# Kernel tuning notes

Hardware: AMD Instinct MI355X
Metric: run time of the kernel (lower is better)

## Reference

```python
import jax, jax.numpy as jnp
import numpy as np

DIM_Q = 512
DIM_K = 512
DIM_V = 512
NUM_HEADS = 8
B, NQ, NK = 4, 2048, 2048


def _linear_init(key, d_in, d_out):
    kw, kb = jax.random.split(key)
    bound = 1.0 / np.sqrt(d_in)
    W = jax.random.uniform(kw, (d_in, d_out), minval=-bound, maxval=bound, dtype=jnp.float32)
    b = jax.random.uniform(kb, (d_out,), minval=-bound, maxval=bound, dtype=jnp.float32)
    return W, b


def setup_inputs() -> dict:
    key = jax.random.key(0)
    ks = jax.random.split(key, 6)
    Q = jax.random.normal(ks[0], (B, NQ, DIM_Q), dtype=jnp.float32)
    K = jax.random.normal(ks[1], (B, NK, DIM_K), dtype=jnp.float32)
    Wq, bq = _linear_init(ks[2], DIM_Q, DIM_V)
    Wk, bk = _linear_init(ks[3], DIM_K, DIM_V)
    Wv, bv = _linear_init(ks[4], DIM_K, DIM_V)
    Wo, bo = _linear_init(ks[5], DIM_V, DIM_V)
    ln0_g = jnp.ones((DIM_V,), jnp.float32)
    ln0_b = jnp.zeros((DIM_V,), jnp.float32)
    ln1_g = jnp.ones((DIM_V,), jnp.float32)
    ln1_b = jnp.zeros((DIM_V,), jnp.float32)
    return {"Q": Q, "K": K, "Wq": Wq, "bq": bq, "Wk": Wk, "bk": bk,
            "Wv": Wv, "bv": bv, "Wo": Wo, "bo": bo,
            "ln0_g": ln0_g, "ln0_b": ln0_b, "ln1_g": ln1_g, "ln1_b": ln1_b}


def _layer_norm(x, g, b, eps=1e-5):
    mu = jnp.mean(x, axis=-1, keepdims=True)
    var = jnp.mean(jnp.square(x - mu), axis=-1, keepdims=True)
    return (x - mu) * jax.lax.rsqrt(var + eps) * g + b


def reference(Q, K, Wq, bq, Wk, bk, Wv, bv, Wo, bo, ln0_g, ln0_b, ln1_g, ln1_b):
    h = NUM_HEADS
    dh = DIM_V // h
    q = Q @ Wq + bq                      # [B, NQ, DIM_V]
    k = K @ Wk + bk                      # [B, NK, DIM_V]
    v = K @ Wv + bv                      # [B, NK, DIM_V]
    qh = q.reshape(B, NQ, h, dh)
    kh = k.reshape(B, NK, h, dh)
    vh = v.reshape(B, NK, h, dh)
    # NOTE: faithful to original — scale by sqrt(dim_V), not sqrt(head_dim)
    scores = jnp.einsum('bqhd,bkhd->bhqk', qh, kh) / jnp.sqrt(jnp.float32(DIM_V))
    A = jax.nn.softmax(scores, axis=-1)  # [B, h, NQ, NK]
    o = jnp.einsum('bhqk,bkhd->bqhd', A, vh) + qh
    H = o.reshape(B, NQ, DIM_V)          # residual with projected Q
    H = _layer_norm(H, ln0_g, ln0_b)
    H = H + jax.nn.relu(H @ Wo + bo)
    H = _layer_norm(H, ln1_g, ln1_b)
    return H
```

## Files before the change

### kernel.cpp

```cpp
#include <hip/hip_runtime.h>

typedef float f32x4 __attribute__((ext_vector_type(4)));
typedef float f32x16 __attribute__((ext_vector_type(16)));
typedef __bf16 bf16x8 __attribute__((ext_vector_type(8)));
typedef unsigned short u16;
typedef unsigned int u32;
typedef u16 u16x8 __attribute__((ext_vector_type(8)));
typedef u16 u16x4 __attribute__((ext_vector_type(4)));
typedef u32 u32x4 __attribute__((ext_vector_type(4)));

#define SCALE2F (0.044194173824159216f * 1.4426950408889634f)
#define UNSCALE (1.0f / SCALE2F)

__device__ __forceinline__ u16 f2bf(float x){ return __builtin_bit_cast(u16, (__bf16)x); }
__device__ __forceinline__ float bf2f(u16 h){ unsigned u = ((unsigned)h) << 16; return __builtin_bit_cast(float, u); }
__device__ __forceinline__ int swz(int r, int byteInRow){ return (r*128 + byteInRow) ^ ((r & 7) << 4); }
__device__ __forceinline__ void gload16(const void* g, void* l) {
  __builtin_amdgcn_global_load_lds(
      (const __attribute__((address_space(1))) void*)g,
      (__attribute__((address_space(3))) void*)l, 16, 0, 0);
}
__device__ __forceinline__ u32 cvtpk(float lo, float hi_) {
  u32 r;
  asm("v_cvt_pk_bf16_f32 %0, %1, %2" : "=v"(r) : "v"(lo), "v"(hi_));
  return r;
}
__device__ __forceinline__ void swap32(u32 &a, u32 &b) {
  asm("v_permlane32_swap_b32 %0, %1" : "+v"(a), "+v"(b));
}

#define MFMA(a,b,c)   __builtin_amdgcn_mfma_f32_16x16x32_bf16((a),(b),(c),0,0,0)
#define MFMA32(a,b,c) __builtin_amdgcn_mfma_f32_32x32x16_bf16((a),(b),(c),0,0,0)

__global__ __launch_bounds__(256) void wprep_k(
    const float* __restrict__ W0, const float* __restrict__ W1,
    const float* __restrict__ W2, const float* __restrict__ W3,
    u16* __restrict__ wt)
{
  __shared__ float tile[64][68];
  const float* Ws[4] = {W0, W1, W2, W3};
  const float* W = Ws[blockIdx.z];
  const float sc = (blockIdx.z == 0) ? SCALE2F : 1.0f;
  u16* out = wt + (size_t)blockIdx.z * 512 * 512;
  int k0 = blockIdx.x * 64, n0 = blockIdx.y * 64;
  int t = threadIdx.x;
  #pragma unroll
  for (int i = 0; i < 2; ++i) {
    int c = t + i*256; int r = c >> 3, k8 = c & 7;
    const float* src = W + (size_t)(k0 + r)*512 + n0 + k8*8;
    *(f32x4*)&tile[r][k8*8]     = *(const f32x4*)src;
    *(f32x4*)&tile[r][k8*8 + 4] = *(const f32x4*)(src + 4);
  }
  __syncthreads();
  #pragma unroll
  for (int i = 0; i < 2; ++i) {
    int c = t + i*256; int r = c >> 3, k8 = c & 7;
    u16x8 h;
    #pragma unroll
    for (int j = 0; j < 8; ++j) h[j] = f2bf(tile[k8*8 + j][r] * sc);
    *(u16x8*)(out + (size_t)(n0 + r)*512 + k0 + k8*8) = h;
  }
}

__global__ __launch_bounds__(512) void proj2_k(
    const float* __restrict__ Qin, const float* __restrict__ Kin,
    const u16* __restrict__ wt,
    const float* __restrict__ bq, const float* __restrict__ bk, const float* __restrict__ bv,
    u16* __restrict__ qbuf, u16* __restrict__ kbuf, u16* __restrict__ vt)
{
  __shared__ __align__(16) u16 lA[2][64*64];
  __shared__ __align__(16) u16 lB0[2][128*64];
  __shared__ __align__(16) u16 lB1[2][128*64];
  int z = blockIdx.z;
  const float* A     = z ? Kin : Qin;
  const u16*   Bt0   = wt + (size_t)(z ? 1 : 0) * 262144;
  const u16*   Bt1   = wt + (size_t)2 * 262144;
  const float* bias0 = z ? bk : bq;
  const float bscale = z ? 1.0f : SCALE2F;
  int row0 = blockIdx.x * 64, col0 = blockIdx.y * 128;
  int t = threadIdx.x, lane = t & 63, wid = t >> 6;
  int wr = wid >> 2, wc = wid & 3;
  int l15 = lane & 15, lg = lane >> 4;
  int ar = t >> 3, ak8 = t & 7;
  int br = t >> 3;
  int bsrc = (((t & 7) << 4) ^ ((br & 7) << 4)) >> 1;
  const float* Arow = A + (size_t)row0 * 512;
  const u16*   B0row = Bt0 + (size_t)col0 * 512;
  const u16*   B1row = Bt1 + (size_t)col0 * 512;

  f32x4 acc0[2][2] = {}, acc1[2][2] = {};

  #pragma unroll
  for (int i = 0; i < 2; ++i)
    gload16(B0row + (size_t)(br + i*64)*512 + bsrc, (char*)lB0[0] + i*8192 + t*16);
  if (z) {
    #pragma unroll
    for (int i = 0; i < 2; ++i)
      gload16(B1row + (size_t)(br + i*64)*512 + bsrc, (char*)lB1[0] + i*8192 + t*16);
  }
  {
    const float* src = Arow + (size_t)ar*512 + ak8*8;
    f32x4 x0 = *(const f32x4*)src;
    f32x4 x1 = *(const f32x4*)(src + 4);
    u16x8 h;
    #pragma unroll
    for (int j = 0; j < 4; ++j) { h[j] = f2bf(x0[j]); h[j+4] = f2bf(x1[j]); }
    *(u16x8*)((char*)lA[0] + swz(ar, ak8*16)) = h;
  }
  __syncthreads();

  int cur = 0;
  for (int k0 = 0; k0 < 512; k0 += 64) {
    bool pf = (k0 + 64 < 512);
    f32x4 px0, px1;
    if (pf) {
      #pragma unroll
      for (int i = 0; i < 2; ++i)
        gload16(B0row + (size_t)(br + i*64)*512 + k0 + 64 + bsrc, (char*)lB0[cur^1] + i*8192 + t*16);
      if (z) {
        #pragma unroll
        for (int i = 0; i < 2; ++i)
          gload16(B1row + (size_t)(br + i*64)*512 + k0 + 64 + bsrc, (char*)lB1[cur^1] + i*8192 + t*16);
      }
      const float* src = Arow + (size_t)ar*512 + k0 + 64 + ak8*8;
      px0 = *(const f32x4*)src;
      px1 = *(const f32x4*)(src + 4);
    }
    const char* lAc = (const char*)lA[cur];
    const char* lB0c = (const char*)lB0[cur];
    const char* lB1c = (const char*)lB1[cur];
    #pragma unroll
    for (int ks = 0; ks < 2; ++ks) {
      bf16x8 af[2], b0f[2], b1f[2];
      #pragma unroll
      for (int m = 0; m < 2; ++m)
        af[m] = *(const bf16x8*)(lAc + swz(wr*32 + m*16 + l15, ks*64 + lg*16));
      #pragma unroll
      for (int n = 0; n < 2; ++n) {
        int rb = wc*32 + n*16 + l15;
        b0f[n] = *(const bf16x8*)(lB0c + swz(rb, ks*64 + lg*16));
        if (z) b1f[n] = *(const bf16x8*)(lB1c + swz(rb, ks*64 + lg*16));
      }
      #pragma unroll
      for (int m = 0; m < 2; ++m)
        #pragma unroll
        for (int n = 0; n < 2; ++n) {
          acc0[m][n] = MFMA(af[m], b0f[n], acc0[m][n]);
          if (z) acc1[m][n] = MFMA(af[m], b1f[n], acc1[m][n]);
        }
    }
    if (pf) {
      u16x8 h;
      #pragma unroll
      for (int j = 0; j < 4; ++j) { h[j] = f2bf(px0[j]); h[j+4] = f2bf(px1[j]); }
      *(u16x8*)((char*)lA[cur^1] + swz(ar, ak8*16)) = h;
    }
    __syncthreads();
    cur ^= 1;
  }

  u16* out0 = z ? kbuf : qbuf;
  #pragma unroll
  for (int m = 0; m < 2; ++m) {
    int rowg = row0 + wr*32 + m*16 + lg*4;
    #pragma unroll
    for (int n = 0; n < 2; ++n) {
      int colg = col0 + wc*32 + n*16 + l15;
      float bvv = bias0[colg] * bscale;
      #pragma unroll
      for (int r = 0; r < 4; ++r)
        out0[(size_t)(rowg + r)*512 + colg] = f2bf(acc0[m][n][r] + bvv);
    }
  }
  if (z) {
    #pragma unroll
    for (int m = 0; m < 2; ++m) {
      int rowg = row0 + wr*32 + m*16 + lg*4;
      int b = rowg >> 11, ntok = rowg & 2047;
      #pragma unroll
      for (int n = 0; n < 2; ++n) {
        int colg = col0 + wc*32 + n*16 + l15;
        float bvv = bv[colg];
        u16x4 hv;
        #pragma unroll
        for (int r = 0; r < 4; ++r) hv[r] = f2bf(acc1[m][n][r] + bvv);
        *(u16x4*)(vt + ((size_t)b*512 + colg)*2048 + ntok) = hv;
      }
    }
  }
}

__global__ __launch_bounds__(512) void gemmo_k(
    const u16* __restrict__ A, const u16* __restrict__ Bt,
    const float* __restrict__ bias, u16* __restrict__ outb,
    const u16* __restrict__ resid)
{
  __shared__ __align__(16) u16 lA[2][64*64];
  __shared__ __align__(16) u16 lB[2][128*64];
  int row0 = blockIdx.x * 64, col0 = blockIdx.y * 128;
  int t = threadIdx.x, lane = t & 63, wid = t >> 6;
  int wr = wid >> 2, wc = wid & 3;
  int l15 = lane & 15, lg = lane >> 4;
  int ar = t >> 3;
  int asrc = (((t & 7) << 4) ^ ((ar & 7) << 4)) >> 1;
  const u16* Arow = A + (size_t)row0 * 512;
  const u16* Brow = Bt + (size_t)col0 * 512;
  f32x4 acc[2][2] = {};

  gload16(Arow + (size_t)ar*512 + asrc, (char*)lA[0] + t*16);
  #pragma unroll
  for (int i = 0; i < 2; ++i)
    gload16(Brow + (size_t)(ar + i*64)*512 + asrc, (char*)lB[0] + i*8192 + t*16);
  __syncthreads();

  int cur = 0;
  for (int k0 = 0; k0 < 512; k0 += 64) {
    if (k0 + 64 < 512) {
      gload16(Arow + (size_t)ar*512 + k0 + 64 + asrc, (char*)lA[cur^1] + t*16);
      #pragma unroll
      for (int i = 0; i < 2; ++i)
        gload16(Brow + (size_t)(ar + i*64)*512 + k0 + 64 + asrc, (char*)lB[cur^1] + i*8192 + t*16);
    }
    const char* lAc = (const char*)lA[cur];
    const char* lBc = (const char*)lB[cur];
    #pragma unroll
    for (int ks = 0; ks < 2; ++ks) {
      bf16x8 af[2], bfv[2];
      #pragma unroll
      for (int m = 0; m < 2; ++m)
        af[m] = *(const bf16x8*)(lAc + swz(wr*32 + m*16 + l15, ks*64 + lg*16));
      #pragma unroll
      for (int n = 0; n < 2; ++n)
        bfv[n] = *(const bf16x8*)(lBc + swz(wc*32 + n*16 + l15, ks*64 + lg*16));
      #pragma unroll
      for (int m = 0; m < 2; ++m)
        #pragma unroll
        for (int n = 0; n < 2; ++n)
          acc[m][n] = MFMA(af[m], bfv[n], acc[m][n]);
    }
    __syncthreads();
    cur ^= 1;
  }
  #pragma unroll
  for (int m = 0; m < 2; ++m) {
    int rowg = row0 + wr*32 + m*16 + lg*4;
    #pragma unroll
    for (int n = 0; n < 2; ++n) {
      int colg = col0 + wc*32 + n*16 + l15;
      float bvv = bias[colg];
      #pragma unroll
      for (int r = 0; r < 4; ++r) {
        size_t idx = (size_t)(rowg + r)*512 + colg;
        outb[idx] = f2bf(bf2f(resid[idx]) + fmaxf(acc[m][n][r] + bvv, 0.0f));
      }
    }
  }
}

__device__ __forceinline__ void mk_pb(const f32x16& s, float& ps, bf16x8& f0, bf16x8& f1) {
  float p[16];
  #pragma unroll
  for (int r = 0; r < 16; ++r) p[r] = __builtin_amdgcn_exp2f(s[r]);
  float t0 = (p[0] + p[1])  + (p[2] + p[3]);
  float t1 = (p[4] + p[5])  + (p[6] + p[7]);
  float t2 = (p[8] + p[9])  + (p[10] + p[11]);
  float t3 = (p[12] + p[13]) + (p[14] + p[15]);
  ps += (t0 + t1) + (t2 + t3);
  u32 a0 = cvtpk(p[0],  p[1]),  b0 = cvtpk(p[4],  p[5]);
  u32 a1 = cvtpk(p[2],  p[3]),  b1 = cvtpk(p[6],  p[7]);
  swap32(a0, b0); swap32(a1, b1);
  u32 a2 = cvtpk(p[8],  p[9]),  b2 = cvtpk(p[12], p[13]);
  u32 a3 = cvtpk(p[10], p[11]), b3 = cvtpk(p[14], p[15]);
  swap32(a2, b2); swap32(a3, b3);
  u32x4 w0 = {a0, a1, b0, b1};
  u32x4 w1 = {a2, a3, b2, b3};
  f0 = __builtin_bit_cast(bf16x8, w0);
  f1 = __builtin_bit_cast(bf16x8, w1);
}

__global__ __launch_bounds__(512, 4) void attn_k(
    const u16* __restrict__ qb, const u16* __restrict__ kb,
    const u16* __restrict__ vt, u16* __restrict__ ob)
{
  __shared__ __align__(16) char smem[65536];

  int t = threadIdx.x, lane = t & 63, wid = t >> 6;
  int bh = blockIdx.y, b = bh >> 3, h = bh & 7;
  int half = wid >> 2;
  int qw = wid & 3;
  int q0 = blockIdx.x * 128 + qw * 32;
  int l31 = lane & 31, hi = lane >> 5;

  const u16* kbase = kb + ((size_t)b*2048)*512 + h*64;
  const u16* vbase = vt + ((size_t)b*512 + h*64)*2048;

  int sr = t >> 3;
  int ssrc = ((t & 7) ^ (sr & 7)) << 3;

#define LKB(hf, bf) (smem + ((hf)*2 + (bf))*8192)
#define LVB(hf, bf) (smem + 32768 + ((hf)*2 + (bf))*8192)
#define STAGE(buf, off)                                                           \
  gload16(kbase + (size_t)((off) + sr)*512 + ssrc,        LKB(0,buf) + t*16);     \
  gload16(kbase + (size_t)((off) + 1024 + sr)*512 + ssrc, LKB(1,buf) + t*16);     \
  gload16(vbase + (size_t)sr*2048 + (off) + ssrc,         LVB(0,buf) + t*16);     \
  gload16(vbase + (size_t)sr*2048 + (off) + 1024 + ssrc,  LVB(1,buf) + t*16);

  bf16x8 aq[4];
  {
    const u16* qp = qb + ((size_t)(b*2048 + q0 + l31))*512 + h*64 + hi*8;
    #pragma unroll
    for (int ks = 0; ks < 4; ++ks) aq[ks] = *(const bf16x8*)(qp + ks*16);
  }

  f32x16 acc[2] = {};
  float ps = 0.0f;

  STAGE(0, 0);
  __syncthreads();

  int cur = 0;
  for (int i = 0; i < 16; ++i) {
    if (i + 1 < 16) { STAGE(cur^1, (i+1)*64); }
    const char* lKc = LKB(half, cur);
    const char* lVc = LVB(half, cur);
    bf16x8 pb[4];
    #pragma unroll
    for (int n = 0; n < 2; ++n) {
      f32x16 s = {};
      #pragma unroll
      for (int ks = 0; ks < 4; ++ks) {
        bf16x8 kf = *(const bf16x8*)(lKc + swz(n*32 + l31, ks*32 + hi*16));
        s = MFMA32(kf, aq[ks], s);
      }
      mk_pb(s, ps, pb[2*n], pb[2*n+1]);
    }
    #pragma unroll
    for (int m = 0; m < 2; ++m)
      #pragma unroll
      for (int ks = 0; ks < 4; ++ks) {
        bf16x8 vf = *(const bf16x8*)(lVc + swz(m*32 + l31, ks*32 + hi*16));
        acc[m] = MFMA32(vf, pb[ks], acc[m]);
      }
    __syncthreads();
    cur ^= 1;
  }
#undef STAGE

  ps += __shfl_xor(ps, 32, 64);
  float* cb = (float*)smem;
  if (half == 1) {
    float* dst = cb + qw * 2208;
    #pragma unroll
    for (int m = 0; m < 2; ++m)
      #pragma unroll
      for (int rq = 0; rq < 4; ++rq) {
        f32x4 v = {acc[m][rq*4], acc[m][rq*4+1], acc[m][rq*4+2], acc[m][rq*4+3]};
        *(f32x4*)(dst + l31*68 + m*32 + rq*8 + hi*4) = v;
      }
    if (hi == 0) dst[2176 + l31] = ps;
  }
  __syncthreads();
  if (half == 0) {
    const float* src = cb + qw * 2208;
    float inv = 1.0f / (ps + src[2176 + l31]);
    u16* obase = ob + ((size_t)(b*2048 + q0 + l31))*512 + h*64;
    const u16* qrb = qb + ((size_t)(b*2048 + q0 + l31))*512 + h*64;
    #pragma unroll
    for (int m = 0; m < 2; ++m)
      #pragma unroll
      for (int rq = 0; rq < 4; ++rq) {
        f32x4 other = *(const f32x4*)(src + l31*68 + m*32 + rq*8 + hi*4);
        u16x4 qr4 = *(const u16x4*)(qrb + m*32 + rq*8 + hi*4);
        u16x4 o4;
        #pragma unroll
        for (int e = 0; e < 4; ++e)
          o4[e] = f2bf((acc[m][rq*4 + e] + other[e])*inv + bf2f(qr4[e])*UNSCALE);
        *(u16x4*)(obase + m*32 + rq*8 + hi*4) = o4;
      }
  }
}

template<int OUT_BF16>
__global__ __launch_bounds__(256) void ln_k(
    const u16* __restrict__ x, const float* __restrict__ gam,
    const float* __restrict__ bet, float* __restrict__ yf, u16* __restrict__ yh)
{
  int t = threadIdx.x, lane = t & 63, w = t >> 6;
  size_t row = (size_t)blockIdx.x * 4 + w;
  u16x8 xv = *(const u16x8*)(x + row*512 + lane*8);
  float v[8];
  #pragma unroll
  for (int j = 0; j < 8; ++j) v[j] = bf2f(xv[j]);
  float s = 0.0f, ss = 0.0f;
  #pragma unroll
  for (int j = 0; j < 8; ++j) { s += v[j]; ss += v[j]*v[j]; }
  #pragma unroll
  for (int m = 1; m < 64; m <<= 1) { s += __shfl_xor(s, m, 64); ss += __shfl_xor(ss, m, 64); }
  float mu = s * (1.0f/512.0f);
  float var = ss * (1.0f/512.0f) - mu*mu;
  float rs = rsqrtf(var + 1e-5f);
  const float* gp = gam + lane*8;
  const float* bp = bet + lane*8;
  f32x4 g0 = *(const f32x4*)gp, g1 = *(const f32x4*)(gp + 4);
  f32x4 b0 = *(const f32x4*)bp, b1 = *(const f32x4*)(bp + 4);
  if (OUT_BF16) {
    u16x8 hv;
    #pragma unroll
    for (int j = 0; j < 4; ++j) {
      hv[j]   = f2bf((v[j]   - mu)*rs*g0[j] + b0[j]);
      hv[j+4] = f2bf((v[j+4] - mu)*rs*g1[j] + b1[j]);
    }
    *(u16x8*)(yh + row*512 + lane*8) = hv;
  } else {
    f32x4 o0, o1;
    #pragma unroll
    for (int j = 0; j < 4; ++j) {
      o0[j] = (v[j]   - mu)*rs*g0[j] + b0[j];
      o1[j] = (v[j+4] - mu)*rs*g1[j] + b1[j];
    }
    float* yp = yf + row*512 + lane*8;
    *(f32x4*)yp = o0;
    *(f32x4*)(yp + 4) = o1;
  }
}

extern "C" void kernel_launch(void* const* d_in, const int* in_sizes, int n_in,
                              void* d_out, int out_size, void* d_ws, size_t ws_size,
                              hipStream_t stream)
{
  const float* Q   = (const float*)d_in[0];
  const float* K   = (const float*)d_in[1];
  const float* Wq  = (const float*)d_in[2];
  const float* bq  = (const float*)d_in[3];
  const float* Wk  = (const float*)d_in[4];
  const float* bk  = (const float*)d_in[5];
  const float* Wv  = (const float*)d_in[6];
  const float* bv  = (const float*)d_in[7];
  const float* Wo  = (const float*)d_in[8];
  const float* bo  = (const float*)d_in[9];
  const float* g0  = (const float*)d_in[10];
  const float* b0  = (const float*)d_in[11];
  const float* g1  = (const float*)d_in[12];
  const float* b1  = (const float*)d_in[13];

  char* ws = (char*)d_ws;
  u16*   wt    = (u16*)(ws + 0);
  u16*   qbuf  = (u16*)(ws + (2u<<20));
  u16*   kbuf  = (u16*)(ws + (10u<<20));
  u16*   vt    = (u16*)(ws + (18u<<20));
  u16*   ob    = (u16*)(ws + (26u<<20));
  u16*   Hbuf  = (u16*)(ws + (34u<<20));
  u16*   Gb    = (u16*)(ws + (42u<<20));

  wprep_k<<<dim3(8, 8, 4), 256, 0, stream>>>(Wq, Wk, Wv, Wo, wt);
  proj2_k<<<dim3(128, 4, 2), 512, 0, stream>>>(Q, K, wt, bq, bk, bv, qbuf, kbuf, vt);
  attn_k<<<dim3(16, 32), 512, 0, stream>>>(qbuf, kbuf, vt, ob);
  ln_k<1><<<2048, 256, 0, stream>>>(ob, g0, b0, nullptr, Hbuf);
  gemmo_k<<<dim3(128, 4), 512, 0, stream>>>(Hbuf, wt + 3*262144, bo, Gb, Hbuf);
  ln_k<0><<<2048, 256, 0, stream>>>(Gb, g1, b1, (float*)d_out, nullptr);
}
```

Measured before the change: 97.91 us.

## Fuse LayerNorm0, output GEMM with ReLU residual, and LayerNorm1 into one kernel

```diff
diff --git a/kernel.cpp b/kernel.cpp
--- a/kernel.cpp
+++ b/kernel.cpp
@@ -190,73 +190,6 @@
   }
 }
 
-__global__ __launch_bounds__(512) void gemmo_k(
-    const u16* __restrict__ A, const u16* __restrict__ Bt,
-    const float* __restrict__ bias, u16* __restrict__ outb,
-    const u16* __restrict__ resid)
-{
-  __shared__ __align__(16) u16 lA[2][64*64];
-  __shared__ __align__(16) u16 lB[2][128*64];
-  int row0 = blockIdx.x * 64, col0 = blockIdx.y * 128;
-  int t = threadIdx.x, lane = t & 63, wid = t >> 6;
-  int wr = wid >> 2, wc = wid & 3;
-  int l15 = lane & 15, lg = lane >> 4;
-  int ar = t >> 3;
-  int asrc = (((t & 7) << 4) ^ ((ar & 7) << 4)) >> 1;
-  const u16* Arow = A + (size_t)row0 * 512;
-  const u16* Brow = Bt + (size_t)col0 * 512;
-  f32x4 acc[2][2] = {};
-
-  gload16(Arow + (size_t)ar*512 + asrc, (char*)lA[0] + t*16);
-  #pragma unroll
-  for (int i = 0; i < 2; ++i)
-    gload16(Brow + (size_t)(ar + i*64)*512 + asrc, (char*)lB[0] + i*8192 + t*16);
-  __syncthreads();
-
-  int cur = 0;
-  for (int k0 = 0; k0 < 512; k0 += 64) {
-    if (k0 + 64 < 512) {
-      gload16(Arow + (size_t)ar*512 + k0 + 64 + asrc, (char*)lA[cur^1] + t*16);
-      #pragma unroll
-      for (int i = 0; i < 2; ++i)
-        gload16(Brow + (size_t)(ar + i*64)*512 + k0 + 64 + asrc, (char*)lB[cur^1] + i*8192 + t*16);
-    }
-    const char* lAc = (const char*)lA[cur];
-    const char* lBc = (const char*)lB[cur];
-    #pragma unroll
-    for (int ks = 0; ks < 2; ++ks) {
-      bf16x8 af[2], bfv[2];
-      #pragma unroll
-      for (int m = 0; m < 2; ++m)
-        af[m] = *(const bf16x8*)(lAc + swz(wr*32 + m*16 + l15, ks*64 + lg*16));
-      #pragma unroll
-      for (int n = 0; n < 2; ++n)
-        bfv[n] = *(const bf16x8*)(lBc + swz(wc*32 + n*16 + l15, ks*64 + lg*16));
-      #pragma unroll
-      for (int m = 0; m < 2; ++m)
-        #pragma unroll
-        for (int n = 0; n < 2; ++n)
-          acc[m][n] = MFMA(af[m], bfv[n], acc[m][n]);
-    }
-    __syncthreads();
-    cur ^= 1;
-  }
-  #pragma unroll
-  for (int m = 0; m < 2; ++m) {
-    int rowg = row0 + wr*32 + m*16 + lg*4;
-    #pragma unroll
-    for (int n = 0; n < 2; ++n) {
-      int colg = col0 + wc*32 + n*16 + l15;
-      float bvv = bias[colg];
-      #pragma unroll
-      for (int r = 0; r < 4; ++r) {
-        size_t idx = (size_t)(rowg + r)*512 + colg;
-        outb[idx] = f2bf(bf2f(resid[idx]) + fmaxf(acc[m][n][r] + bvv, 0.0f));
-      }
-    }
-  }
-}
-
 __device__ __forceinline__ void mk_pb(const f32x16& s, float& ps, bf16x8& f0, bf16x8& f1) {
   float p[16];
   #pragma unroll
@@ -380,47 +313,161 @@
   }
 }
 
-template<int OUT_BF16>
-__global__ __launch_bounds__(256) void ln_k(
-    const u16* __restrict__ x, const float* __restrict__ gam,
-    const float* __restrict__ bet, float* __restrict__ yf, u16* __restrict__ yh)
+__global__ __launch_bounds__(512) void tail_k(
+    const u16* __restrict__ ob, const u16* __restrict__ Bt,
+    const float* __restrict__ bo,
+    const float* __restrict__ g0, const float* __restrict__ b0,
+    const float* __restrict__ g1, const float* __restrict__ b1,
+    float* __restrict__ out)
 {
-  int t = threadIdx.x, lane = t & 63, w = t >> 6;
-  size_t row = (size_t)blockIdx.x * 4 + w;
-  u16x8 xv = *(const u16x8*)(x + row*512 + lane*8);
-  float v[8];
-  #pragma unroll
-  for (int j = 0; j < 8; ++j) v[j] = bf2f(xv[j]);
-  float s = 0.0f, ss = 0.0f;
-  #pragma unroll
-  for (int j = 0; j < 8; ++j) { s += v[j]; ss += v[j]*v[j]; }
-  #pragma unroll
-  for (int m = 1; m < 64; m <<= 1) { s += __shfl_xor(s, m, 64); ss += __shfl_xor(ss, m, 64); }
-  float mu = s * (1.0f/512.0f);
-  float var = ss * (1.0f/512.0f) - mu*mu;
-  float rs = rsqrtf(var + 1e-5f);
-  const float* gp = gam + lane*8;
-  const float* bp = bet + lane*8;
-  f32x4 g0 = *(const f32x4*)gp, g1 = *(const f32x4*)(gp + 4);
-  f32x4 b0 = *(const f32x4*)bp, b1 = *(const f32x4*)(bp + 4);
-  if (OUT_BF16) {
-    u16x8 hv;
+  __shared__ __align__(16) u16 lA[2][32*64];
+  __shared__ __align__(16) u16 lB[2][512*64];
+  __shared__ float mu0[32], rs0[32], mu1[32], rs1[32];
+  __shared__ float ps1[32][8], ss1[32][8];
+
+  int row0 = blockIdx.x * 32;
+  int t = threadIdx.x, lane = t & 63, wid = t >> 6;
+  int l15 = lane & 15, lg = lane >> 4;
+
+  {
+    int r = t >> 4, c0 = (t & 15) * 32;
+    const u16* xp = ob + (size_t)(row0 + r)*512 + c0;
+    float s = 0.0f, ss = 0.0f;
     #pragma unroll
     for (int j = 0; j < 4; ++j) {
-      hv[j]   = f2bf((v[j]   - mu)*rs*g0[j] + b0[j]);
-      hv[j+4] = f2bf((v[j+4] - mu)*rs*g1[j] + b1[j]);
-    }
-    *(u16x8*)(yh + row*512 + lane*8) = hv;
-  } else {
-    f32x4 o0, o1;
-    #pragma unroll
-    for (int j = 0; j < 4; ++j) {
-      o0[j] = (v[j]   - mu)*rs*g0[j] + b0[j];
-      o1[j] = (v[j+4] - mu)*rs*g1[j] + b1[j];
-    }
-    float* yp = yf + row*512 + lane*8;
-    *(f32x4*)yp = o0;
-    *(f32x4*)(yp + 4) = o1;
+      u16x8 v = *(const u16x8*)(xp + j*8);
+      #pragma unroll
+      for (int e = 0; e < 8; ++e) { float f = bf2f(v[e]); s += f; ss += f*f; }
+    }
+    #pragma unroll
+    for (int m = 1; m < 16; m <<= 1) { s += __shfl_xor(s, m, 64); ss += __shfl_xor(ss, m, 64); }
+    if ((t & 15) == 0) {
+      float mu = s * (1.0f/512.0f);
+      float var = ss * (1.0f/512.0f) - mu*mu;
+      mu0[r] = mu; rs0[r] = rsqrtf(var + 1e-5f);
+    }
+  }
+  __syncthreads();
+
+  int ar = t >> 3, ak8 = t & 7;
+  int br = t >> 3;
+  int bsrc = ((t & 7) ^ (br & 7)) << 3;
+
+  auto stageA = [&](int buf, int k0) {
+    if (t < 256) {
+      u16x8 x = *(const u16x8*)(ob + (size_t)(row0 + ar)*512 + k0 + ak8*8);
+      f32x4 gv0 = *(const f32x4*)(g0 + k0 + ak8*8);
+      f32x4 gv1 = *(const f32x4*)(g0 + k0 + ak8*8 + 4);
+      f32x4 bv0 = *(const f32x4*)(b0 + k0 + ak8*8);
+      f32x4 bv1 = *(const f32x4*)(b0 + k0 + ak8*8 + 4);
+      float mu = mu0[ar], rs = rs0[ar];
+      u16x8 h;
+      #pragma unroll
+      for (int j = 0; j < 4; ++j) {
+        h[j]   = f2bf((bf2f(x[j])   - mu)*rs*gv0[j] + bv0[j]);
+        h[j+4] = f2bf((bf2f(x[j+4]) - mu)*rs*gv1[j] + bv1[j]);
+      }
+      *(u16x8*)((char*)lA[buf] + swz(ar, ak8*16)) = h;
+    }
+  };
+
+  #pragma unroll
+  for (int i = 0; i < 8; ++i)
+    gload16(Bt + (size_t)(br + i*64)*512 + bsrc, (char*)lB[0] + i*8192 + t*16);
+  stageA(0, 0);
+  __syncthreads();
+
+  f32x4 acc[2][4] = {};
+  int cur = 0;
+  for (int k0 = 0; k0 < 512; k0 += 64) {
+    if (k0 + 64 < 512) {
+      #pragma unroll
+      for (int i = 0; i < 8; ++i)
+        gload16(Bt + (size_t)(br + i*64)*512 + k0 + 64 + bsrc, (char*)lB[cur^1] + i*8192 + t*16);
+      stageA(cur^1, k0 + 64);
+    }
+    const char* lAc = (const char*)lA[cur];
+    const char* lBc = (const char*)lB[cur];
+    #pragma unroll
+    for (int ks = 0; ks < 2; ++ks) {
+      bf16x8 af[2], bfv[4];
+      #pragma unroll
+      for (int m = 0; m < 2; ++m)
+        af[m] = *(const bf16x8*)(lAc + swz(m*16 + l15, ks*64 + lg*16));
+      #pragma unroll
+      for (int n = 0; n < 4; ++n)
+        bfv[n] = *(const bf16x8*)(lBc + swz(wid*64 + n*16 + l15, ks*64 + lg*16));
+      #pragma unroll
+      for (int m = 0; m < 2; ++m)
+        #pragma unroll
+        for (int n = 0; n < 4; ++n)
+          acc[m][n] = MFMA(af[m], bfv[n], acc[m][n]);
+    }
+    __syncthreads();
+    cur ^= 1;
+  }
+
+  float Gv[2][4][4];
+  float sp[2][4] = {}, ssp[2][4] = {};
+  #pragma unroll
+  for (int n = 0; n < 4; ++n) {
+    int colg = wid*64 + n*16 + l15;
+    float bov = bo[colg];
+    float g0c = g0[colg], b0c = b0[colg];
+    #pragma unroll
+    for (int m = 0; m < 2; ++m) {
+      #pragma unroll
+      for (int rr = 0; rr < 4; ++rr) {
+        int rit = m*16 + lg*4 + rr;
+        float H = (bf2f(ob[(size_t)(row0 + rit)*512 + colg]) - mu0[rit])*rs0[rit]*g0c + b0c;
+        float G = H + fmaxf(acc[m][n][rr] + bov, 0.0f);
+        Gv[m][n][rr] = G;
+        sp[m][rr] += G;
+        ssp[m][rr] += G*G;
+      }
+    }
+  }
+  #pragma unroll
+  for (int msk = 1; msk < 16; msk <<= 1)
+    #pragma unroll
+    for (int m = 0; m < 2; ++m)
+      #pragma unroll
+      for (int rr = 0; rr < 4; ++rr) {
+        sp[m][rr]  += __shfl_xor(sp[m][rr],  msk, 64);
+        ssp[m][rr] += __shfl_xor(ssp[m][rr], msk, 64);
+      }
+  if (l15 == 0) {
+    #pragma unroll
+    for (int m = 0; m < 2; ++m)
+      #pragma unroll
+      for (int rr = 0; rr < 4; ++rr) {
+        int rit = m*16 + lg*4 + rr;
+        ps1[rit][wid] = sp[m][rr];
+        ss1[rit][wid] = ssp[m][rr];
+      }
+  }
+  __syncthreads();
+  if (t < 32) {
+    float s = 0.0f, ss = 0.0f;
+    #pragma unroll
+    for (int w = 0; w < 8; ++w) { s += ps1[t][w]; ss += ss1[t][w]; }
+    float mu = s * (1.0f/512.0f);
+    float var = ss * (1.0f/512.0f) - mu*mu;
+    mu1[t] = mu; rs1[t] = rsqrtf(var + 1e-5f);
+  }
+  __syncthreads();
+  #pragma unroll
+  for (int n = 0; n < 4; ++n) {
+    int colg = wid*64 + n*16 + l15;
+    float g1c = g1[colg], b1c = b1[colg];
+    #pragma unroll
+    for (int m = 0; m < 2; ++m)
+      #pragma unroll
+      for (int rr = 0; rr < 4; ++rr) {
+        int rit = m*16 + lg*4 + rr;
+        out[(size_t)(row0 + rit)*512 + colg] =
+            (Gv[m][n][rr] - mu1[rit])*rs1[rit]*g1c + b1c;
+      }
   }
 }
 
@@ -449,13 +496,9 @@
   u16*   kbuf  = (u16*)(ws + (10u<<20));
   u16*   vt    = (u16*)(ws + (18u<<20));
   u16*   ob    = (u16*)(ws + (26u<<20));
-  u16*   Hbuf  = (u16*)(ws + (34u<<20));
-  u16*   Gb    = (u16*)(ws + (42u<<20));
 
   wprep_k<<<dim3(8, 8, 4), 256, 0, stream>>>(Wq, Wk, Wv, Wo, wt);
   proj2_k<<<dim3(128, 4, 2), 512, 0, stream>>>(Q, K, wt, bq, bk, bv, qbuf, kbuf, vt);
   attn_k<<<dim3(16, 32), 512, 0, stream>>>(qbuf, kbuf, vt, ob);
-  ln_k<1><<<2048, 256, 0, stream>>>(ob, g0, b0, nullptr, Hbuf);
-  gemmo_k<<<dim3(128, 4), 512, 0, stream>>>(Hbuf, wt + 3*262144, bo, Gb, Hbuf);
-  ln_k<0><<<2048, 256, 0, stream>>>(Gb, g1, b1, (float*)d_out, nullptr);
-}
+  tail_k<<<256, 512, 0, stream>>>(ob, wt + 3*262144, bo, g0, b0, g1, b1, (float*)d_out);
+}
```

Result: faster. 95.60 us (-2.4%).
